# Performance work log

Hardware: AMD Instinct MI355X
Metric: run time of the kernel (lower is better)

The kernel has to match this reference:

```python
import jax, jax.numpy as jnp
import numpy as np
import math

B, L, IN_F, OUT_F = 16, 4096, 384, 384
SCALE = 1.0 / math.sqrt(IN_F)
EPS = 1e-8


def setup_inputs() -> dict:
    key = jax.random.key(0)
    k1, k2, k3 = jax.random.split(key, 3)
    return {
        "Efou": jax.random.normal(k1, (B, L, IN_F), dtype=jnp.float32),
        "y": jax.random.normal(k2, (B, IN_F), dtype=jnp.float32),
        "weight": jax.random.normal(k3, (1, OUT_F, IN_F), dtype=jnp.float32),
    }


def reference(Efou, y, weight):
    b, size_patch, in_f = Efou.shape
    out_f = weight.shape[1]
    # per-sample weight modulation: [B, out, in]
    w = SCALE * weight * y[:, None, :]
    # demodulation
    dconf = jax.lax.rsqrt(jnp.sum(w * w, axis=2) + EPS)  # [B, out]
    w = w * dconf[:, :, None]
    # Faithful raw reshape of [B, L, in] buffer to [B, in, L] layout (NOT a transpose),
    # matching torch's Efou.reshape(1, B*in, L) + grouped conv1d with kernel size 1.
    Xr = Efou.reshape(b, in_f, size_patch)
    out = jnp.einsum("boi,bip->bop", w, Xr)  # [B, out, L]
    # Faithful raw view of (B*out, L) buffer as (B, L, out)
    return out.reshape(b, size_patch, out_f)
```

## Files before the change

kernel.cpp:

```cpp
#include <hip/hip_runtime.h>
#include <hip/hip_bf16.h>
#include <stdint.h>

#define Bn 16
#define Ln 4096
#define KF 384
#define OF 384

#define BM 128
#define BN 128
#define BK 64
#define LDX 72

static constexpr float kScale = 0.051031036307982884f;

typedef __attribute__((ext_vector_type(4))) float f32x4;
typedef __attribute__((ext_vector_type(2))) float f32x2;
typedef __attribute__((ext_vector_type(8))) short short8;
typedef __attribute__((ext_vector_type(4))) float floatx4;
typedef __attribute__((ext_vector_type(4))) unsigned int uint4v;

__device__ __forceinline__ void gl_lds16(const void* g, void* l) {
  __builtin_amdgcn_global_load_lds(
      (const __attribute__((address_space(1))) unsigned int*)g,
      (__attribute__((address_space(3))) unsigned int*)l, 16, 0, 0);
}

__device__ __forceinline__ unsigned int f2bf_bits(float f) {
  union { float f; unsigned int u; } v;
  v.f = f;
  return (v.u + 0x7FFFu + ((v.u >> 16) & 1u)) >> 16;
}
__device__ __forceinline__ unsigned int pack2bf(float lo, float hi) {
  return f2bf_bits(lo) | (f2bf_bits(hi) << 16);
}

__device__ __forceinline__ unsigned int cvt_pk_bf16(float lo, float hi) {
  unsigned int r;
  asm("v_cvt_pk_bf16_f32 %0, %1, %2" : "=v"(r) : "v"(lo), "v"(hi));
  return r;
}

__global__ __launch_bounds__(256) void modw_kernel(const float* __restrict__ weight,
                                                   const float* __restrict__ y,
                                                   unsigned short* __restrict__ wmod) {
  int t = threadIdx.x;
  int wv = t >> 6, lane = t & 63;
  int row = blockIdx.x * 4 + wv;
  int b = row / OF, o = row % OF;
  const float* wr = weight + o * KF;
  const float* yr = y + b * KF;
  float vals[6];
  float ss = 0.f;
#pragma unroll
  for (int j = 0; j < 3; ++j) {
    int k = (lane + 64 * j) * 2;
    f32x2 wvv = *(const f32x2*)(wr + k);
    f32x2 yv = *(const f32x2*)(yr + k);
    float t0 = kScale * wvv[0] * yv[0];
    float t1 = kScale * wvv[1] * yv[1];
    vals[2 * j] = t0;
    vals[2 * j + 1] = t1;
    ss += t0 * t0 + t1 * t1;
  }
#pragma unroll
  for (int off = 32; off >= 1; off >>= 1) ss += __shfl_xor(ss, off, 64);
  float d = rsqrtf(ss + 1e-8f);
  unsigned short* orow = wmod + row * KF;
#pragma unroll
  for (int j = 0; j < 3; ++j) {
    int k = (lane + 64 * j) * 2;
    *(unsigned int*)(orow + k) = pack2bf(vals[2 * j] * d, vals[2 * j + 1] * d);
  }
}

__global__ __launch_bounds__(256, 3) void gemm_kernel(const float* __restrict__ X,
                                                      const unsigned short* __restrict__ Wm,
                                                      float* __restrict__ out) {
  __shared__ unsigned short sA[2][BM * BK];
  __shared__ unsigned short sX[2][BN * LDX];

  int flat = blockIdx.x;
  int logical = (flat & 7) * 192 + (flat >> 3);
  int mt = logical % 3;
  int nt = (logical / 3) & 31;
  int b = logical / 96;

  int t = threadIdx.x;
  int wave = t >> 6, lane = t & 63;
  int quad = lane >> 4;

  const float* Xb = X + b * (KF * Ln);
  const unsigned short* Wb = Wm + (b * OF + mt * BM) * KF;
  int pbase = nt * BN;

  floatx4 acc[4][4] = {};

  int i31 = t & 31;
  int p0 = i31 * 4;
  int kr0 = (t >> 5) * 8;
  int kr0s = (((t >> 5) ^ (i31 & 7)) * 8);
  int arow = (wave >> 1) * 64 + (lane & 15);
  int brow = (wave & 1) * 64 + (lane & 15);
  int asw = lane & 7;
  int xsw = ((lane & 15) >> 2);

  int aoff[4], asrc_row[4], asrc_c[4];
#pragma unroll
  for (int j = 0; j < 4; ++j) {
    int boff = wave * 4096 + j * 1024 + lane * 16;
    int row = boff >> 7;
    int cp = (boff >> 4) & 7;
    aoff[j] = boff;
    asrc_row[j] = row;
    asrc_c[j] = (cp ^ (row & 7)) * 8;
  }

  f32x4 xv[8];
  unsigned int wv4[4][4];

#pragma unroll
  for (int j = 0; j < 4; ++j)
    gl_lds16(Wb + asrc_row[j] * KF + 0 + asrc_c[j], (char*)sA[0] + aoff[j]);
  {
    const float* xsrc = Xb + (0 + kr0) * Ln + pbase + p0;
#pragma unroll
    for (int i = 0; i < 8; ++i) xv[i] = *(const f32x4*)(xsrc + i * Ln);
#pragma unroll
    for (int j = 0; j < 4; ++j)
#pragma unroll
      for (int i = 0; i < 4; ++i)
        wv4[j][i] = cvt_pk_bf16(xv[2 * i][j], xv[2 * i + 1][j]);
#pragma unroll
    for (int j = 0; j < 4; ++j)
      *(uint4v*)(&sX[0][(p0 + j) * LDX + kr0s]) = *(uint4v*)wv4[j];
  }
  __syncthreads();
  {
    const float* xsrc = Xb + (BK + kr0) * Ln + pbase + p0;
#pragma unroll
    for (int i = 0; i < 8; ++i) xv[i] = *(const f32x4*)(xsrc + i * Ln);
  }

#pragma unroll
  for (int kc = 0; kc < 6; ++kc) {
    int cur = kc & 1;
    if (kc < 5) {
      int k0n = (kc + 1) * BK;
#pragma unroll
      for (int j = 0; j < 4; ++j)
        gl_lds16(Wb + asrc_row[j] * KF + k0n + asrc_c[j], (char*)sA[cur ^ 1] + aoff[j]);
    }
#pragma unroll
    for (int s = 0; s < 2; ++s) {
      short8 af[4], bf[4];
#pragma unroll
      for (int mi = 0; mi < 4; ++mi) {
        int ca = (((s << 2) | quad) ^ asw) * 8;
        af[mi] = *(const short8*)(&sA[cur][(arow + mi * 16) * BK + ca]);
      }
#pragma unroll
      for (int ni = 0; ni < 4; ++ni) {
        int cx = (((s << 2) | quad) ^ (((ni & 1) << 2) | xsw)) * 8;
        bf[ni] = *(const short8*)(&sX[cur][(brow + ni * 16) * LDX + cx]);
      }
      __builtin_amdgcn_s_setprio(1);
#pragma unroll
      for (int mi = 0; mi < 4; ++mi)
#pragma unroll
        for (int ni = 0; ni < 4; ++ni)
          acc[mi][ni] = __builtin_amdgcn_mfma_f32_16x16x32_bf16(af[mi], bf[ni], acc[mi][ni], 0, 0, 0);
      __builtin_amdgcn_s_setprio(0);
    }
    if (kc < 5) {
#pragma unroll
      for (int j = 0; j < 4; ++j)
#pragma unroll
        for (int i = 0; i < 4; ++i)
          wv4[j][i] = cvt_pk_bf16(xv[2 * i][j], xv[2 * i + 1][j]);
#pragma unroll
      for (int j = 0; j < 4; ++j)
        *(uint4v*)(&sX[cur ^ 1][(p0 + j) * LDX + kr0s]) = *(uint4v*)wv4[j];
      __syncthreads();
      if (kc < 4) {
        const float* xsrc = Xb + ((kc + 2) * BK + kr0) * Ln + pbase + p0;
#pragma unroll
        for (int i = 0; i < 8; ++i) xv[i] = *(const f32x4*)(xsrc + i * Ln);
      }
    }
  }

  float* outb = out + (b * OF + mt * BM) * Ln + pbase;
  int col = lane & 15;
#pragma unroll
  for (int mi = 0; mi < 4; ++mi) {
    int ob = (wave >> 1) * 64 + mi * 16 + quad * 4;
#pragma unroll
    for (int ni = 0; ni < 4; ++ni) {
      int p = (wave & 1) * 64 + ni * 16 + col;
#pragma unroll
      for (int r = 0; r < 4; ++r) outb[(ob + r) * Ln + p] = acc[mi][ni][r];
    }
  }
}

extern "C" void kernel_launch(void* const* d_in, const int* in_sizes, int n_in,
                              void* d_out, int out_size, void* d_ws, size_t ws_size,
                              hipStream_t stream) {
  const float* Efou = (const float*)d_in[0];
  const float* y = (const float*)d_in[1];
  const float* weight = (const float*)d_in[2];
  float* out = (float*)d_out;
  unsigned short* wmod = (unsigned short*)d_ws;

  modw_kernel<<<(Bn * OF) / 4, 256, 0, stream>>>(weight, y, wmod);
  gemm_kernel<<<Bn * (OF / BM) * (Ln / BN), 256, 0, stream>>>(Efou, wmod, out);
}
```

Before: 204.1 us.

## Process two N-tiles per block with continuous K pipeline across tiles

Each GEMM block now handles two consecutive 128-column output tiles, so the grid is halved. The double-buffered K loop runs over 12 chunks, and the prefetch of the next tile's first chunks overlaps with the epilogue of the previous tile. This removes per-block prologue and pipeline fill cost and lets output stores overlap with loads. The trade-off is fewer blocks (768 instead of 1536), which reduces parallelism, and mid-loop stores that could add register pressure.

```diff
diff --git a/kernel.cpp b/kernel.cpp
--- a/kernel.cpp
+++ b/kernel.cpp
@@ -11,6 +11,8 @@
 #define BN 128
 #define BK 64
 #define LDX 72
+#define NPT 2
+#define NCH 12
 
 static constexpr float kScale = 0.051031036307982884f;
 
@@ -81,10 +83,10 @@
   __shared__ unsigned short sX[2][BN * LDX];
 
   int flat = blockIdx.x;
-  int logical = (flat & 7) * 192 + (flat >> 3);
+  int logical = (flat & 7) * 96 + (flat >> 3);
   int mt = logical % 3;
-  int nt = (logical / 3) & 31;
-  int b = logical / 96;
+  int ntg = (logical / 3) & 15;
+  int b = logical / 48;
 
   int t = threadIdx.x;
   int wave = t >> 6, lane = t & 63;
@@ -92,7 +94,7 @@
 
   const float* Xb = X + b * (KF * Ln);
   const unsigned short* Wb = Wm + (b * OF + mt * BM) * KF;
-  int pbase = nt * BN;
+  int pbase = ntg * (BN * NPT);
 
   floatx4 acc[4][4] = {};
 
@@ -143,10 +145,10 @@
   }
 
 #pragma unroll
-  for (int kc = 0; kc < 6; ++kc) {
-    int cur = kc & 1;
-    if (kc < 5) {
-      int k0n = (kc + 1) * BK;
+  for (int c = 0; c < NCH; ++c) {
+    int cur = c & 1;
+    if (c < NCH - 1) {
+      int k0n = ((c + 1) % 6) * BK;
 #pragma unroll
       for (int j = 0; j < 4; ++j)
         gl_lds16(Wb + asrc_row[j] * KF + k0n + asrc_c[j], (char*)sA[cur ^ 1] + aoff[j]);
@@ -172,7 +174,30 @@
           acc[mi][ni] = __builtin_amdgcn_mfma_f32_16x16x32_bf16(af[mi], bf[ni], acc[mi][ni], 0, 0, 0);
       __builtin_amdgcn_s_setprio(0);
     }
-    if (kc < 5) {
+    if ((c % 6) == 5) {
+      int pt = c / 6;
+      float* outb = out + (b * OF + mt * BM) * Ln + pbase + pt * BN;
+      int col = lane & 15;
+#pragma unroll
+      for (int mi = 0; mi < 4; ++mi) {
+        int ob = (wave >> 1) * 64 + mi * 16 + quad * 4;
+#pragma unroll
+        for (int ni = 0; ni < 4; ++ni) {
+          int p = (wave & 1) * 64 + ni * 16 + col;
+#pragma unroll
+          for (int r = 0; r < 4; ++r) outb[(ob + r) * Ln + p] = acc[mi][ni][r];
+        }
+      }
+      if (c < NCH - 1) {
+#pragma unroll
+        for (int mi = 0; mi < 4; ++mi)
+#pragma unroll
+          for (int ni = 0; ni < 4; ++ni)
+#pragma unroll
+            for (int r = 0; r < 4; ++r) acc[mi][ni][r] = 0.f;
+      }
+    }
+    if (c < NCH - 1) {
 #pragma unroll
       for (int j = 0; j < 4; ++j)
 #pragma unroll
@@ -182,24 +207,13 @@
       for (int j = 0; j < 4; ++j)
         *(uint4v*)(&sX[cur ^ 1][(p0 + j) * LDX + kr0s]) = *(uint4v*)wv4[j];
       __syncthreads();
-      if (kc < 4) {
-        const float* xsrc = Xb + ((kc + 2) * BK + kr0) * Ln + pbase + p0;
+      if (c < NCH - 2) {
+        int c2 = c + 2;
+        const float* xsrc =
+            Xb + ((c2 % 6) * BK + kr0) * Ln + pbase + (c2 / 6) * BN + p0;
 #pragma unroll
         for (int i = 0; i < 8; ++i) xv[i] = *(const f32x4*)(xsrc + i * Ln);
       }
-    }
-  }
-
-  float* outb = out + (b * OF + mt * BM) * Ln + pbase;
-  int col = lane & 15;
-#pragma unroll
-  for (int mi = 0; mi < 4; ++mi) {
-    int ob = (wave >> 1) * 64 + mi * 16 + quad * 4;
-#pragma unroll
-    for (int ni = 0; ni < 4; ++ni) {
-      int p = (wave & 1) * 64 + ni * 16 + col;
-#pragma unroll
-      for (int r = 0; r < 4; ++r) outb[(ob + r) * Ln + p] = acc[mi][ni][r];
     }
   }
 }
@@ -214,5 +228,5 @@
   unsigned short* wmod = (unsigned short*)d_ws;
 
   modw_kernel<<<(Bn * OF) / 4, 256, 0, stream>>>(weight, y, wmod);
-  gemm_kernel<<<Bn * (OF / BM) * (Ln / BN), 256, 0, stream>>>(Efou, wmod, out);
-}
+  gemm_kernel<<<Bn * (OF / BM) * (Ln / (BN * NPT)), 256, 0, stream>>>(Efou, wmod, out);
+}
```

Result: slower. 217.7 us (+6.7%).
